# Kernel tuning notes

Hardware: AMD Instinct MI355X
Metric: run time of the kernel (lower is better)

The kernel has to match this reference:

```python
import jax, jax.numpy as jnp
import numpy as np

CS = 64          # chunk_size
CP = CS - 1      # causal_padding
H = 8            # heads
DH = 64          # dim_head
SCALE = DH ** -0.5


def rotate_half(x):
    x1, x2 = jnp.split(x, 2, axis=-1)
    return jnp.concatenate((-x2, x1), axis=-1)


def apply_rope(t, freqs):
    rd = freqs.shape[-1]
    t_rot, t_pass = t[..., :rd], t[..., rd:]
    t_rot = t_rot * jnp.cos(freqs) + rotate_half(t_rot) * jnp.sin(freqs)
    return jnp.concatenate((t_rot, t_pass), axis=-1)


def setup_inputs() -> dict:
    key = jax.random.key(0)
    ks = jax.random.split(key, 10)
    b, n, dim = 4, 4096, 1024
    k_chunks, r, rlen = 64, 2, 128
    inner = H * DH
    return {
        "x": jax.random.normal(ks[0], (b, n, dim), dtype=jnp.float32),
        "context": jax.random.normal(ks[1], (b, k_chunks, r, rlen, dim), dtype=jnp.float32),
        "q_pos_emb": jax.random.normal(ks[2], (1, 1, CS, DH), dtype=jnp.float32),
        "k_pos_emb": jax.random.normal(ks[3], (1, 1, rlen, DH), dtype=jnp.float32),
        "Wq": jax.random.normal(ks[4], (dim, inner), dtype=jnp.float32) * 0.02,
        "Wk": jax.random.normal(ks[5], (dim, inner), dtype=jnp.float32) * 0.02,
        "Wv": jax.random.normal(ks[6], (dim, inner), dtype=jnp.float32) * 0.02,
        "Wo": jax.random.normal(ks[7], (inner, dim), dtype=jnp.float32) * 0.02,
        "bo": jnp.zeros((dim,), dtype=jnp.float32),
        "null_k": jax.random.normal(ks[8], (inner,), dtype=jnp.float32),
        "null_v": jax.random.normal(ks[9], (inner,), dtype=jnp.float32),
    }


def reference(x, context, q_pos_emb, k_pos_emb, Wq, Wk, Wv, Wo, bo, null_k, null_v):
    b, n, dim = x.shape
    _, k_chunks, r, rlen, _ = context.shape
    # causal shift: drop first CP tokens, pad CP zeros at end (F.pad with -CP)
    xs = jnp.pad(x[:, CP:], ((0, 0), (0, CP), (0, 0)))
    seq_index = (n // CS) * CS
    rem = n - seq_index
    xs = xs[:, :seq_index]                                   # [b, k*CS, dim]
    # shift q rope the same way; pad region gets freqs=0 -> identity rotation
    qpe = jnp.pad(q_pos_emb[:, :, CP:], ((0, 0), (0, 0), (0, CP), (0, 0)))
    kpe = jnp.tile(k_pos_emb, (1, 1, r, 1))                  # [1,1,r*rlen,DH]
    bk = b * k_chunks
    xc = xs.reshape(bk, CS, dim)
    ctx = context.reshape(bk, r * rlen, dim)
    # projections -> [bk, h, seq, dh]
    q = (xc @ Wq).reshape(bk, CS, H, DH).transpose(0, 2, 1, 3) * SCALE
    k = (ctx @ Wk).reshape(bk, r * rlen, H, DH).transpose(0, 2, 1, 3)
    v = (ctx @ Wv).reshape(bk, r * rlen, H, DH).transpose(0, 2, 1, 3)
    q = apply_rope(q, qpe)
    k = apply_rope(k, kpe)
    # null kv prepend
    nk = jnp.broadcast_to(null_k.reshape(1, H, 1, DH), (bk, H, 1, DH))
    nv = jnp.broadcast_to(null_v.reshape(1, H, 1, DH), (bk, H, 1, DH))
    k = jnp.concatenate((nk, k), axis=2)
    v = jnp.concatenate((nv, v), axis=2)
    sim = jnp.einsum('bhid,bhjd->bhij', q, k)
    attn = jax.nn.softmax(sim, axis=-1)
    o = jnp.einsum('bhij,bhjd->bhid', attn, v)
    o = o.transpose(0, 2, 1, 3).reshape(bk, CS, H * DH)
    o = o @ Wo + bo                                          # [bk, CS, dim]
    o = o.reshape(b, k_chunks * CS, dim)
    # unshift: pad CP zeros at front, trim CP - rem from end
    o = jnp.concatenate(
        (jnp.zeros((b, CP, dim), o.dtype), o[:, :k_chunks * CS - CP + rem]), axis=1)
    return o
```

## Files before the change

### kernel.cpp

```cpp
#include <hip/hip_runtime.h>


#define DEV __device__ __forceinline__

typedef __bf16 bf16x8 __attribute__((ext_vector_type(8)));
typedef float f32x4 __attribute__((ext_vector_type(4)));

DEV unsigned short f2bf(float f) {
  union { float f; unsigned int u; } v; v.f = f;
  unsigned int u = v.u;
  unsigned int r = (u + 0x7FFFu + ((u >> 16) & 1u)) >> 16;
  return (unsigned short)r;
}
DEV float bf2f(unsigned short h) {
  union { unsigned int u; float f; } v; v.u = ((unsigned int)h) << 16;
  return v.f;
}

DEV void ldst16(const void* g, void* l) {
  __builtin_amdgcn_global_load_lds(
      (const __attribute__((address_space(1))) void*)g,
      (__attribute__((address_space(3))) void*)l, 16, 0, 0);
}


__global__ __launch_bounds__(256) void cast_ctx_k(const float* __restrict__ src,
                                                  unsigned short* __restrict__ dst) {
  size_t i = ((size_t)blockIdx.x * 256 + threadIdx.x) * 8;
  float4 a = *(const float4*)(src + i);
  float4 b = *(const float4*)(src + i + 4);
  union { uint4 v; unsigned short s[8]; } u;
  u.s[0] = f2bf(a.x); u.s[1] = f2bf(a.y); u.s[2] = f2bf(a.z); u.s[3] = f2bf(a.w);
  u.s[4] = f2bf(b.x); u.s[5] = f2bf(b.y); u.s[6] = f2bf(b.z); u.s[7] = f2bf(b.w);
  *(uint4*)(dst + i) = u.v;
}

__global__ __launch_bounds__(256) void cast_x_k(const float* __restrict__ x,
                                                unsigned short* __restrict__ xq) {
  size_t flat = ((size_t)blockIdx.x * 256 + threadIdx.x) * 8;
  int row = (int)(flat >> 10);
  int c = (int)(flat & 1023);
  int b = row >> 12, p = row & 4095;
  union { uint4 v; unsigned short s[8]; } u;
  if (p <= 4032) {
    const float* sp = x + (((size_t)(b << 12) + p + 63) << 10) + c;
    float4 a = *(const float4*)sp;
    float4 d = *(const float4*)(sp + 4);
    u.s[0] = f2bf(a.x); u.s[1] = f2bf(a.y); u.s[2] = f2bf(a.z); u.s[3] = f2bf(a.w);
    u.s[4] = f2bf(d.x); u.s[5] = f2bf(d.y); u.s[6] = f2bf(d.z); u.s[7] = f2bf(d.w);
  } else {
    #pragma unroll
    for (int e = 0; e < 8; ++e) u.s[e] = 0;
  }
  *(uint4*)(xq + flat) = u.v;
}

__global__ __launch_bounds__(256) void transpose_w_k(const float* __restrict__ W,
                                                     unsigned short* __restrict__ Wt,
                                                     int kbits, int N, float scale) {
  int idx = blockIdx.x * 256 + threadIdx.x;
  int K = 1 << kbits;
  int k = idx & (K - 1), n = idx >> kbits;
  Wt[idx] = f2bf(W[(size_t)k * N + n] * scale);
}

__global__ __launch_bounds__(256) void rope_tables_k(const float* __restrict__ qpe,
                                                     const float* __restrict__ kpe,
                                                     float* __restrict__ ck, float* __restrict__ sk,
                                                     float* __restrict__ cq, float* __restrict__ sq) {
  int t = blockIdx.x * 256 + threadIdx.x;
  float f = kpe[t];
  ck[t] = cosf(f);
  sk[t] = sinf(f);
  if (t < 64) {
    float g = qpe[63 * 64 + t];
    cq[t] = cosf(g);
    sq[t] = sinf(g);
  }
}

__global__ __launch_bounds__(256) void rope_k_k(unsigned short* __restrict__ kb,
                                                const float* __restrict__ ck,
                                                const float* __restrict__ sk) {
  size_t t = (size_t)blockIdx.x * 256 + threadIdx.x;
  int m = (int)(t >> 8);
  int rest = (int)(t & 255);
  int h = rest >> 5, dp = rest & 31;
  size_t base = (size_t)m * 512 + h * 64;
  int fi = (m & 127) * 64 + dp;
  float v0 = bf2f(kb[base + dp]);
  float v1 = bf2f(kb[base + dp + 32]);
  float c0 = ck[fi], s0 = sk[fi], c1 = ck[fi + 32], s1 = sk[fi + 32];
  kb[base + dp] = f2bf(v0 * c0 - v1 * s0);
  kb[base + dp + 32] = f2bf(v1 * c1 + v0 * s1);
}

__global__ __launch_bounds__(256) void rope_q_k(unsigned short* __restrict__ qb,
                                                const float* __restrict__ cq,
                                                const float* __restrict__ sq) {
  int t = blockIdx.x * 256 + threadIdx.x;
  int bc = t >> 8, rest = t & 255, h = rest >> 5, dp = rest & 31;
  size_t base = (size_t)(bc * 64) * 512 + h * 64;
  float v0 = bf2f(qb[base + dp]);
  float v1 = bf2f(qb[base + dp + 32]);
  qb[base + dp] = f2bf(v0 * cq[dp] - v1 * sq[dp]);
  qb[base + dp + 32] = f2bf(v1 * cq[dp + 32] + v0 * sq[dp + 32]);
}

__global__ __launch_bounds__(256) void zero_rows_k(float* __restrict__ out) {
  int b = blockIdx.x / 63, rr = blockIdx.x % 63;
  float4 z = {0.f, 0.f, 0.f, 0.f};
  *(float4*)(out + (((size_t)(b * 4096 + rr)) << 10) + threadIdx.x * 4) = z;
}

__global__ __launch_bounds__(256) void gemm_bt(const unsigned short* __restrict__ A,
                                               const unsigned short* __restrict__ B0,
                                               const unsigned short* __restrict__ B1,
                                               unsigned short* __restrict__ C0,
                                               unsigned short* __restrict__ C1,
                                               int M, int N, int K) {
  __shared__ unsigned short As[128 * 64];
  __shared__ unsigned short Bs[128 * 64];
  const unsigned short* B = blockIdx.z ? B1 : B0;
  unsigned short* C = blockIdx.z ? C1 : C0;
  int m0 = blockIdx.x * 128, n0 = blockIdx.y * 128;
  int tid = threadIdx.x, w = tid >> 6, lane = tid & 63;
  int wm = (w & 1) * 64, wn = (w >> 1) * 64;
  int Lrow = lane >> 3, Lc = lane & 7;
  int srcC = Lc ^ (Lrow & 7);

  f32x4 acc[4][4] = {};

  for (int k0 = 0; k0 < K; k0 += 64) {
    #pragma unroll
    for (int q = 0; q < 4; ++q) {
      int t = w * 4 + q;
      ldst16(A + (size_t)(m0 + t * 8 + Lrow) * K + (k0 + srcC * 8), (char*)As + t * 1024);
      ldst16(B + (size_t)(n0 + t * 8 + Lrow) * K + (k0 + srcC * 8), (char*)Bs + t * 1024);
    }
    __syncthreads();
    #pragma unroll
    for (int k32 = 0; k32 < 2; ++k32) {
      int c = k32 * 4 + (lane >> 4);
      bf16x8 af[4], bfr[4];
      #pragma unroll
      for (int mt = 0; mt < 4; ++mt) {
        int m = wm + mt * 16 + (lane & 15);
        af[mt] = *(const bf16x8*)((const char*)As + m * 128 + (c ^ (m & 7)) * 16);
      }
      #pragma unroll
      for (int nt = 0; nt < 4; ++nt) {
        int n = wn + nt * 16 + (lane & 15);
        bfr[nt] = *(const bf16x8*)((const char*)Bs + n * 128 + (c ^ (n & 7)) * 16);
      }
      #pragma unroll
      for (int mt = 0; mt < 4; ++mt)
        #pragma unroll
        for (int nt = 0; nt < 4; ++nt)
          acc[mt][nt] = __builtin_amdgcn_mfma_f32_16x16x32_bf16(af[mt], bfr[nt], acc[mt][nt], 0, 0, 0);
    }
    __syncthreads();
  }
  #pragma unroll
  for (int mt = 0; mt < 4; ++mt)
    #pragma unroll
    for (int nt = 0; nt < 4; ++nt)
      #pragma unroll
      for (int r = 0; r < 4; ++r) {
        int m = m0 + wm + mt * 16 + (lane >> 4) * 4 + r;
        int n = n0 + wn + nt * 16 + (lane & 15);
        C[(size_t)m * N + n] = f2bf(acc[mt][nt][r]);
      }
}

__global__ __launch_bounds__(256) void gemm_out(const unsigned short* __restrict__ A,
                                                const unsigned short* __restrict__ B,
                                                const float* __restrict__ bias,
                                                float* __restrict__ out,
                                                int M, int N, int K) {
  __shared__ unsigned short As[128 * 64];
  __shared__ unsigned short Bs[128 * 64];
  int m0 = blockIdx.x * 128, n0 = blockIdx.y * 128;
  int tid = threadIdx.x, w = tid >> 6, lane = tid & 63;
  int wm = (w & 1) * 64, wn = (w >> 1) * 64;
  int Lrow = lane >> 3, Lc = lane & 7;
  int srcC = Lc ^ (Lrow & 7);

  f32x4 acc[4][4] = {};

  for (int k0 = 0; k0 < K; k0 += 64) {
    #pragma unroll
    for (int q = 0; q < 4; ++q) {
      int t = w * 4 + q;
      ldst16(A + (size_t)(m0 + t * 8 + Lrow) * K + (k0 + srcC * 8), (char*)As + t * 1024);
      ldst16(B + (size_t)(n0 + t * 8 + Lrow) * K + (k0 + srcC * 8), (char*)Bs + t * 1024);
    }
    __syncthreads();
    #pragma unroll
    for (int k32 = 0; k32 < 2; ++k32) {
      int c = k32 * 4 + (lane >> 4);
      bf16x8 af[4], bfr[4];
      #pragma unroll
      for (int mt = 0; mt < 4; ++mt) {
        int m = wm + mt * 16 + (lane & 15);
        af[mt] = *(const bf16x8*)((const char*)As + m * 128 + (c ^ (m & 7)) * 16);
      }
      #pragma unroll
      for (int nt = 0; nt < 4; ++nt) {
        int n = wn + nt * 16 + (lane & 15);
        bfr[nt] = *(const bf16x8*)((const char*)Bs + n * 128 + (c ^ (n & 7)) * 16);
      }
      #pragma unroll
      for (int mt = 0; mt < 4; ++mt)
        #pragma unroll
        for (int nt = 0; nt < 4; ++nt)
          acc[mt][nt] = __builtin_amdgcn_mfma_f32_16x16x32_bf16(af[mt], bfr[nt], acc[mt][nt], 0, 0, 0);
    }
    __syncthreads();
  }
  #pragma unroll
  for (int mt = 0; mt < 4; ++mt)
    #pragma unroll
    for (int nt = 0; nt < 4; ++nt)
      #pragma unroll
      for (int r = 0; r < 4; ++r) {
        int m = m0 + wm + mt * 16 + (lane >> 4) * 4 + r;
        int n = n0 + wn + nt * 16 + (lane & 15);
        int b = m >> 12, t = m & 4095;
        if (t <= 4032)
          out[((size_t)((b << 12) + t + 63)) * N + n] = acc[mt][nt][r] + bias[n];
      }
}

__global__ __launch_bounds__(256) void attn_kernel(const unsigned short* __restrict__ qb,
                                                   const unsigned short* __restrict__ kb,
                                                   const unsigned short* __restrict__ vb,
                                                   const float* __restrict__ nullk,
                                                   const float* __restrict__ nullv,
                                                   unsigned short* __restrict__ ob) {
  __shared__ unsigned short qs[64 * 64];
  __shared__ unsigned short ks[256 * 64];
  __shared__ unsigned short ps[64 * 256];
  __shared__ float rnull[64];
  __shared__ float rsum[64];
  int bc = blockIdx.x, h = blockIdx.y;
  int tid = threadIdx.x, w = tid >> 6, lane = tid & 63;
  int Lrow = lane >> 3, Lc = lane & 7, srcC = Lc ^ (Lrow & 7);

  #pragma unroll
  for (int q8 = 0; q8 < 2; ++q8) {
    int t = w * 2 + q8;
    ldst16(qb + (size_t)(bc * 64 + t * 8 + Lrow) * 512 + h * 64 + srcC * 8, (char*)qs + t * 1024);
  }
  #pragma unroll
  for (int q8 = 0; q8 < 8; ++q8) {
    int t = w * 8 + q8;
    ldst16(kb + (size_t)(bc * 256 + t * 8 + Lrow) * 512 + h * 64 + srcC * 8, (char*)ks + t * 1024);
  }
  __syncthreads();

  {
    int rl = lane >> 2, part = lane & 3;
    int row = w * 16 + rl;
    float s = 0.f;
    #pragma unroll
    for (int e = 0; e < 16; ++e) {
      int d = part * 16 + e;
      unsigned short qv = *(const unsigned short*)((const char*)qs + row * 128 +
                                                   (((d >> 3) ^ (row & 7)) * 16) + (d & 7) * 2);
      s += bf2f(qv) * nullk[h * 64 + d];
    }
    s += __shfl_xor(s, 1);
    s += __shfl_xor(s, 2);
    if (part == 0) rnull[row] = s;
  }

  f32x4 acc[16] = {};
  #pragma unroll
  for (int k32 = 0; k32 < 2; ++k32) {
    int c = k32 * 4 + (lane >> 4);
    int m = w * 16 + (lane & 15);
    bf16x8 a = *(const bf16x8*)((const char*)qs + m * 128 + (c ^ (m & 7)) * 16);
    #pragma unroll
    for (int nt = 0; nt < 16; ++nt) {
      int n = nt * 16 + (lane & 15);
      bf16x8 b = *(const bf16x8*)((const char*)ks + n * 128 + (c ^ (n & 7)) * 16);
      acc[nt] = __builtin_amdgcn_mfma_f32_16x16x32_bf16(a, b, acc[nt], 0, 0, 0);
    }
  }

  int g = lane >> 4;
  #pragma unroll
  for (int r = 0; r < 4; ++r) {
    int row = w * 16 + g * 4 + r;
    float mx = -3.0e38f;
    #pragma unroll
    for (int nt = 0; nt < 16; ++nt) mx = fmaxf(mx, acc[nt][r]);
    mx = fmaxf(mx, __shfl_xor(mx, 1));
    mx = fmaxf(mx, __shfl_xor(mx, 2));
    mx = fmaxf(mx, __shfl_xor(mx, 4));
    mx = fmaxf(mx, __shfl_xor(mx, 8));
    float ns = rnull[row];
    float mm = fmaxf(mx, ns);
    float s = 0.f;
    #pragma unroll
    for (int nt = 0; nt < 16; ++nt) {
      float p = __expf(acc[nt][r] - mm);
      acc[nt][r] = p;
      s += p;
    }
    s += __shfl_xor(s, 1);
    s += __shfl_xor(s, 2);
    s += __shfl_xor(s, 4);
    s += __shfl_xor(s, 8);
    float en = __expf(ns - mm);
    s += en;
    if ((lane & 15) == 0) {
      rsum[row] = s;
      rnull[row] = en;
    }
  }

  #pragma unroll
  for (int nt = 0; nt < 16; ++nt)
    #pragma unroll
    for (int r = 0; r < 4; ++r) {
      int row = w * 16 + g * 4 + r;
      int col = nt * 16 + (lane & 15);
      *(unsigned short*)((char*)ps + row * 512 + (((col >> 3) ^ (row & 7)) * 16) + (col & 7) * 2) =
          f2bf(acc[nt][r]);
    }
  __syncthreads();

  {
    unsigned short* vt = ks;
    const unsigned short* vg = vb + (size_t)(bc * 256 + tid) * 512 + h * 64;
    #pragma unroll
    for (int cc = 0; cc < 8; ++cc) {
      uint4 raw = *(const uint4*)(vg + cc * 8);
      union { uint4 v; unsigned short s[8]; } u;
      u.v = raw;
      #pragma unroll
      for (int e = 0; e < 8; ++e) {
        int d = cc * 8 + e;
        *(unsigned short*)((char*)vt + d * 512 + (((tid >> 3) ^ (d & 7)) * 16) + (tid & 7) * 2) = u.s[e];
      }
    }
  }
  __syncthreads();

  f32x4 oacc[4] = {};
  #pragma unroll
  for (int k32 = 0; k32 < 8; ++k32) {
    int c = k32 * 4 + (lane >> 4);
    int m = w * 16 + (lane & 15);
    bf16x8 a = *(const bf16x8*)((const char*)ps + m * 512 + (c ^ (m & 7)) * 16);
    #pragma unroll
    for (int nt = 0; nt < 4; ++nt) {
      int n = nt * 16 + (lane & 15);
      bf16x8 b = *(const bf16x8*)((const char*)ks + n * 512 + (c ^ (n & 7)) * 16);
      oacc[nt] = __builtin_amdgcn_mfma_f32_16x16x32_bf16(a, b, oacc[nt], 0, 0, 0);
    }
  }
  #pragma unroll
  for (int nt = 0; nt < 4; ++nt)
    #pragma unroll
    for (int r = 0; r < 4; ++r) {
      int row = w * 16 + g * 4 + r;
      int d = nt * 16 + (lane & 15);
      float o = oacc[nt][r] + rnull[row] * nullv[h * 64 + d];
      o /= rsum[row];
      ob[((size_t)(bc * 64 + row) * 8 + h) * 64 + d] = f2bf(o);
    }
}

extern "C" void kernel_launch(void* const* d_in, const int* in_sizes, int n_in,
                              void* d_out, int out_size, void* d_ws, size_t ws_size,
                              hipStream_t stream) {
  const float* x = (const float*)d_in[0];
  const float* ctx = (const float*)d_in[1];
  const float* qpe = (const float*)d_in[2];
  const float* kpe = (const float*)d_in[3];
  const float* Wq = (const float*)d_in[4];
  const float* Wk = (const float*)d_in[5];
  const float* Wv = (const float*)d_in[6];
  const float* Wo = (const float*)d_in[7];
  const float* bo = (const float*)d_in[8];
  const float* nk = (const float*)d_in[9];
  const float* nv = (const float*)d_in[10];
  float* out = (float*)d_out;
  char* ws = (char*)d_ws;

  unsigned short* xq   = (unsigned short*)(ws + 0);
  unsigned short* ctxb = (unsigned short*)(ws + 33554432);
  unsigned short* Wqt  = (unsigned short*)(ws + 167772160);
  unsigned short* Wkt  = (unsigned short*)(ws + 168820736);
  unsigned short* Wvt  = (unsigned short*)(ws + 169869312);
  unsigned short* Wot  = (unsigned short*)(ws + 170917888);
  unsigned short* qb   = (unsigned short*)(ws + 171966464);
  unsigned short* kb   = (unsigned short*)(ws + 188743680);
  unsigned short* vb   = (unsigned short*)(ws + 255852544);
  unsigned short* obuf = (unsigned short*)(ws + 322961408);
  float* cosk = (float*)(ws + 339738624);
  float* sink = (float*)(ws + 339771392);
  float* cosq = (float*)(ws + 339804160);
  float* sinq = (float*)(ws + 339804416);

  zero_rows_k<<<252, 256, 0, stream>>>(out);
  cast_ctx_k<<<32768, 256, 0, stream>>>(ctx, ctxb);
  cast_x_k<<<8192, 256, 0, stream>>>(x, xq);
  transpose_w_k<<<2048, 256, 0, stream>>>(Wq, Wqt, 10, 512, 0.125f);
  transpose_w_k<<<2048, 256, 0, stream>>>(Wk, Wkt, 10, 512, 1.0f);
  transpose_w_k<<<2048, 256, 0, stream>>>(Wv, Wvt, 10, 512, 1.0f);
  transpose_w_k<<<2048, 256, 0, stream>>>(Wo, Wot, 9, 1024, 1.0f);
  rope_tables_k<<<32, 256, 0, stream>>>(qpe, kpe, cosk, sink, cosq, sinq);

  gemm_bt<<<dim3(128, 4, 1), 256, 0, stream>>>(xq, Wqt, Wqt, qb, qb, 16384, 512, 1024);
  gemm_bt<<<dim3(512, 4, 2), 256, 0, stream>>>(ctxb, Wkt, Wvt, kb, vb, 65536, 512, 1024);

  rope_q_k<<<256, 256, 0, stream>>>(qb, cosq, sinq);
  rope_k_k<<<65536, 256, 0, stream>>>(kb, cosk, sink);

  attn_kernel<<<dim3(256, 8), 256, 0, stream>>>(qb, kb, vb, nk, nv, obuf);

  gemm_out<<<dim3(128, 8), 256, 0, stream>>>(obuf, Wot, bo, out, 16384, 1024, 512);
}
```

Measured before the change: 813.3 us.

## Fuse RoPE into projection GEMM epilogues and emit transposed V

Merges the prep kernels (weight transposes, rope tables, zeroing) into one launch and the two casts into another. RoPE for Q and K is now applied in the projection GEMM epilogue, which removes the separate read-modify-write passes over kb and qb. The V projection writes a transposed layout through LDS, so the attention kernel can load V^T with async global-to-LDS copies instead of transposing it with scattered shared stores. Block indices are also remapped, with N-tile-fastest ordering in the GEMMs and grouped chunk/head order in attention, to improve L2 reuse. The cost is strided column writes for transposed V and extra cos/sin table lookups in the epilogue.

After: 804.5 us. Within noise of the previous version (-1.1%).

```diff
diff --git a/kernel.cpp b/kernel.cpp
--- a/kernel.cpp
+++ b/kernel.cpp
@@ -23,107 +23,106 @@
       (__attribute__((address_space(3))) void*)l, 16, 0, 0);
 }
 
-
-__global__ __launch_bounds__(256) void cast_ctx_k(const float* __restrict__ src,
-                                                  unsigned short* __restrict__ dst) {
-  size_t i = ((size_t)blockIdx.x * 256 + threadIdx.x) * 8;
-  float4 a = *(const float4*)(src + i);
-  float4 b = *(const float4*)(src + i + 4);
-  union { uint4 v; unsigned short s[8]; } u;
-  u.s[0] = f2bf(a.x); u.s[1] = f2bf(a.y); u.s[2] = f2bf(a.z); u.s[3] = f2bf(a.w);
-  u.s[4] = f2bf(b.x); u.s[5] = f2bf(b.y); u.s[6] = f2bf(b.z); u.s[7] = f2bf(b.w);
-  *(uint4*)(dst + i) = u.v;
-}
-
-__global__ __launch_bounds__(256) void cast_x_k(const float* __restrict__ x,
-                                                unsigned short* __restrict__ xq) {
-  size_t flat = ((size_t)blockIdx.x * 256 + threadIdx.x) * 8;
-  int row = (int)(flat >> 10);
-  int c = (int)(flat & 1023);
-  int b = row >> 12, p = row & 4095;
-  union { uint4 v; unsigned short s[8]; } u;
-  if (p <= 4032) {
-    const float* sp = x + (((size_t)(b << 12) + p + 63) << 10) + c;
-    float4 a = *(const float4*)sp;
-    float4 d = *(const float4*)(sp + 4);
+__global__ __launch_bounds__(256) void prep_k(const float* __restrict__ Wq,
+                                              const float* __restrict__ Wk,
+                                              const float* __restrict__ Wv,
+                                              const float* __restrict__ Wo,
+                                              const float* __restrict__ qpe,
+                                              const float* __restrict__ kpe,
+                                              unsigned short* __restrict__ Wqt,
+                                              unsigned short* __restrict__ Wkt,
+                                              unsigned short* __restrict__ Wvt,
+                                              unsigned short* __restrict__ Wot,
+                                              float* __restrict__ ck, float* __restrict__ sk,
+                                              float* __restrict__ cq, float* __restrict__ sq,
+                                              float* __restrict__ out) {
+  int blk = blockIdx.x;
+  if (blk < 8192) {
+    int idx = blk * 256 + threadIdx.x;
+    int which = idx >> 19;
+    int loc = idx & 524287;
+    if (which < 3) {
+      int k = loc & 1023, n = loc >> 10;
+      const float* W = which == 0 ? Wq : (which == 1 ? Wk : Wv);
+      unsigned short* Wt = which == 0 ? Wqt : (which == 1 ? Wkt : Wvt);
+      float scale = which == 0 ? 0.125f : 1.0f;
+      Wt[loc] = f2bf(W[(size_t)k * 512 + n] * scale);
+    } else {
+      int k = loc & 511, n = loc >> 9;
+      Wot[loc] = f2bf(Wo[(size_t)k * 1024 + n]);
+    }
+  } else if (blk < 8444) {
+    int r = blk - 8192;
+    int b = r / 63, rr = r % 63;
+    float4 z = {0.f, 0.f, 0.f, 0.f};
+    *(float4*)(out + (((size_t)(b * 4096 + rr)) << 10) + threadIdx.x * 4) = z;
+  } else {
+    int t = (blk - 8444) * 256 + threadIdx.x;
+    float f = kpe[t];
+    ck[t] = cosf(f);
+    sk[t] = sinf(f);
+    if (t < 64) {
+      float g = qpe[63 * 64 + t];
+      cq[t] = cosf(g);
+      sq[t] = sinf(g);
+    }
+  }
+}
+
+__global__ __launch_bounds__(256) void cast_k(const float* __restrict__ ctx,
+                                              const float* __restrict__ x,
+                                              unsigned short* __restrict__ ctxb,
+                                              unsigned short* __restrict__ xq) {
+  int blk = blockIdx.x;
+  if (blk < 32768) {
+    size_t i = ((size_t)blk * 256 + threadIdx.x) * 8;
+    float4 a = *(const float4*)(ctx + i);
+    float4 b = *(const float4*)(ctx + i + 4);
+    union { uint4 v; unsigned short s[8]; } u;
     u.s[0] = f2bf(a.x); u.s[1] = f2bf(a.y); u.s[2] = f2bf(a.z); u.s[3] = f2bf(a.w);
-    u.s[4] = f2bf(d.x); u.s[5] = f2bf(d.y); u.s[6] = f2bf(d.z); u.s[7] = f2bf(d.w);
+    u.s[4] = f2bf(b.x); u.s[5] = f2bf(b.y); u.s[6] = f2bf(b.z); u.s[7] = f2bf(b.w);
+    *(uint4*)(ctxb + i) = u.v;
   } else {
-    #pragma unroll
-    for (int e = 0; e < 8; ++e) u.s[e] = 0;
-  }
-  *(uint4*)(xq + flat) = u.v;
-}
-
-__global__ __launch_bounds__(256) void transpose_w_k(const float* __restrict__ W,
-                                                     unsigned short* __restrict__ Wt,
-                                                     int kbits, int N, float scale) {
-  int idx = blockIdx.x * 256 + threadIdx.x;
-  int K = 1 << kbits;
-  int k = idx & (K - 1), n = idx >> kbits;
-  Wt[idx] = f2bf(W[(size_t)k * N + n] * scale);
-}
-
-__global__ __launch_bounds__(256) void rope_tables_k(const float* __restrict__ qpe,
-                                                     const float* __restrict__ kpe,
-                                                     float* __restrict__ ck, float* __restrict__ sk,
-                                                     float* __restrict__ cq, float* __restrict__ sq) {
-  int t = blockIdx.x * 256 + threadIdx.x;
-  float f = kpe[t];
-  ck[t] = cosf(f);
-  sk[t] = sinf(f);
-  if (t < 64) {
-    float g = qpe[63 * 64 + t];
-    cq[t] = cosf(g);
-    sq[t] = sinf(g);
-  }
-}
-
-__global__ __launch_bounds__(256) void rope_k_k(unsigned short* __restrict__ kb,
-                                                const float* __restrict__ ck,
-                                                const float* __restrict__ sk) {
-  size_t t = (size_t)blockIdx.x * 256 + threadIdx.x;
-  int m = (int)(t >> 8);
-  int rest = (int)(t & 255);
-  int h = rest >> 5, dp = rest & 31;
-  size_t base = (size_t)m * 512 + h * 64;
-  int fi = (m & 127) * 64 + dp;
-  float v0 = bf2f(kb[base + dp]);
-  float v1 = bf2f(kb[base + dp + 32]);
-  float c0 = ck[fi], s0 = sk[fi], c1 = ck[fi + 32], s1 = sk[fi + 32];
-  kb[base + dp] = f2bf(v0 * c0 - v1 * s0);
-  kb[base + dp + 32] = f2bf(v1 * c1 + v0 * s1);
-}
-
-__global__ __launch_bounds__(256) void rope_q_k(unsigned short* __restrict__ qb,
-                                                const float* __restrict__ cq,
-                                                const float* __restrict__ sq) {
-  int t = blockIdx.x * 256 + threadIdx.x;
-  int bc = t >> 8, rest = t & 255, h = rest >> 5, dp = rest & 31;
-  size_t base = (size_t)(bc * 64) * 512 + h * 64;
-  float v0 = bf2f(qb[base + dp]);
-  float v1 = bf2f(qb[base + dp + 32]);
-  qb[base + dp] = f2bf(v0 * cq[dp] - v1 * sq[dp]);
-  qb[base + dp + 32] = f2bf(v1 * cq[dp + 32] + v0 * sq[dp + 32]);
-}
-
-__global__ __launch_bounds__(256) void zero_rows_k(float* __restrict__ out) {
-  int b = blockIdx.x / 63, rr = blockIdx.x % 63;
-  float4 z = {0.f, 0.f, 0.f, 0.f};
-  *(float4*)(out + (((size_t)(b * 4096 + rr)) << 10) + threadIdx.x * 4) = z;
-}
-
-__global__ __launch_bounds__(256) void gemm_bt(const unsigned short* __restrict__ A,
-                                               const unsigned short* __restrict__ B0,
-                                               const unsigned short* __restrict__ B1,
-                                               unsigned short* __restrict__ C0,
-                                               unsigned short* __restrict__ C1,
-                                               int M, int N, int K) {
-  __shared__ unsigned short As[128 * 64];
-  __shared__ unsigned short Bs[128 * 64];
-  const unsigned short* B = blockIdx.z ? B1 : B0;
-  unsigned short* C = blockIdx.z ? C1 : C0;
-  int m0 = blockIdx.x * 128, n0 = blockIdx.y * 128;
+    size_t flat = ((size_t)(blk - 32768) * 256 + threadIdx.x) * 8;
+    int row = (int)(flat >> 10);
+    int c = (int)(flat & 1023);
+    int b = row >> 12, p = row & 4095;
+    union { uint4 v; unsigned short s[8]; } u;
+    if (p <= 4032) {
+      const float* sp = x + (((size_t)(b << 12) + p + 63) << 10) + c;
+      float4 a = *(const float4*)sp;
+      float4 d = *(const float4*)(sp + 4);
+      u.s[0] = f2bf(a.x); u.s[1] = f2bf(a.y); u.s[2] = f2bf(a.z); u.s[3] = f2bf(a.w);
+      u.s[4] = f2bf(d.x); u.s[5] = f2bf(d.y); u.s[6] = f2bf(d.z); u.s[7] = f2bf(d.w);
+    } else {
+      #pragma unroll
+      for (int e = 0; e < 8; ++e) u.s[e] = 0;
+    }
+    *(uint4*)(xq + flat) = u.v;
+  }
+}
+
+template <int MODE>
+__global__ __launch_bounds__(256) void gemm_proj(const unsigned short* __restrict__ A,
+                                                 const unsigned short* __restrict__ B0,
+                                                 const unsigned short* __restrict__ B1,
+                                                 unsigned short* __restrict__ out0,
+                                                 unsigned short* __restrict__ out1,
+                                                 const float* __restrict__ ck,
+                                                 const float* __restrict__ sk,
+                                                 const float* __restrict__ cq,
+                                                 const float* __restrict__ sq,
+                                                 int M, int K) {
+  __shared__ unsigned short sh[16384];
+  unsigned short* As = sh;
+  unsigned short* Bs = sh + 8192;
+
+  int id = blockIdx.x;
+  int x, y, z;
+  if (MODE == 0) { y = id & 3; x = id >> 2; z = 0; }
+  else           { y = id & 3; z = (id >> 2) & 1; x = id >> 3; }
+  const unsigned short* B = z ? B1 : B0;
+  int m0 = x * 128, n0 = y * 128;
   int tid = threadIdx.x, w = tid >> 6, lane = tid & 63;
   int wm = (w & 1) * 64, wn = (w >> 1) * 64;
   int Lrow = lane >> 3, Lc = lane & 7;
@@ -161,26 +160,75 @@
     }
     __syncthreads();
   }
-  #pragma unroll
-  for (int mt = 0; mt < 4; ++mt)
-    #pragma unroll
-    for (int nt = 0; nt < 4; ++nt)
+
+  if (MODE == 0) {
+    #pragma unroll
+    for (int mt = 0; mt < 4; ++mt)
+      #pragma unroll
+      for (int nt = 0; nt < 4; ++nt)
+        #pragma unroll
+        for (int r = 0; r < 4; ++r) {
+          int m = m0 + wm + mt * 16 + (lane >> 4) * 4 + r;
+          int n = n0 + wn + nt * 16 + (lane & 15);
+          float val = acc[mt][nt][r];
+          if ((m & 63) == 0) {
+            int d = nt * 16 + (lane & 15);
+            float partner = acc[mt][nt ^ 2][r];
+            val = val * cq[d] + (nt < 2 ? -partner : partner) * sq[d];
+          }
+          out0[(size_t)m * 512 + n] = f2bf(val);
+        }
+  } else if (z == 0) {
+    #pragma unroll
+    for (int mt = 0; mt < 4; ++mt)
       #pragma unroll
       for (int r = 0; r < 4; ++r) {
         int m = m0 + wm + mt * 16 + (lane >> 4) * 4 + r;
-        int n = n0 + wn + nt * 16 + (lane & 15);
-        C[(size_t)m * N + n] = f2bf(acc[mt][nt][r]);
-      }
+        int fib = (m & 127) * 64;
+        #pragma unroll
+        for (int nt = 0; nt < 4; ++nt) {
+          int n = n0 + wn + nt * 16 + (lane & 15);
+          int d = nt * 16 + (lane & 15);
+          float partner = acc[mt][nt ^ 2][r];
+          float val = acc[mt][nt][r] * ck[fib + d] + (nt < 2 ? -partner : partner) * sk[fib + d];
+          out0[(size_t)m * 512 + n] = f2bf(val);
+        }
+      }
+  } else {
+    #pragma unroll
+    for (int mt = 0; mt < 4; ++mt)
+      #pragma unroll
+      for (int nt = 0; nt < 4; ++nt)
+        #pragma unroll
+        for (int r = 0; r < 4; ++r) {
+          int ml = wm + mt * 16 + (lane >> 4) * 4 + r;
+          int nl = wn + nt * 16 + (lane & 15);
+          int mc = ml >> 3, me = ml & 7;
+          *(unsigned short*)((char*)sh + nl * 256 + ((mc ^ (nl & 15)) * 16) + me * 2) =
+              f2bf(acc[mt][nt][r]);
+        }
+    __syncthreads();
+    #pragma unroll
+    for (int i = 0; i < 8; ++i) {
+      int flat = i * 256 + tid;
+      int nl = flat >> 4, mc = flat & 15;
+      uint4 v = *(const uint4*)((const char*)sh + nl * 256 + ((mc ^ (nl & 15)) * 16));
+      *(uint4*)(out1 + (size_t)(n0 + nl) * M + m0 + mc * 8) = v;
+    }
+  }
 }
 
 __global__ __launch_bounds__(256) void gemm_out(const unsigned short* __restrict__ A,
                                                 const unsigned short* __restrict__ B,
                                                 const float* __restrict__ bias,
-                                                float* __restrict__ out,
-                                                int M, int N, int K) {
-  __shared__ unsigned short As[128 * 64];
-  __shared__ unsigned short Bs[128 * 64];
-  int m0 = blockIdx.x * 128, n0 = blockIdx.y * 128;
+                                                float* __restrict__ out) {
+  __shared__ unsigned short sh[16384];
+  unsigned short* As = sh;
+  unsigned short* Bs = sh + 8192;
+  const int K = 512, N = 1024;
+  int id = blockIdx.x;
+  int y = id & 7, x = id >> 3;
+  int m0 = x * 128, n0 = y * 128;
   int tid = threadIdx.x, w = tid >> 6, lane = tid & 63;
   int wm = (w & 1) * 64, wn = (w >> 1) * 64;
   int Lrow = lane >> 3, Lc = lane & 7;
@@ -234,7 +282,7 @@
 
 __global__ __launch_bounds__(256) void attn_kernel(const unsigned short* __restrict__ qb,
                                                    const unsigned short* __restrict__ kb,
-                                                   const unsigned short* __restrict__ vb,
+                                                   const unsigned short* __restrict__ vtg,
                                                    const float* __restrict__ nullk,
                                                    const float* __restrict__ nullv,
                                                    unsigned short* __restrict__ ob) {
@@ -243,7 +291,9 @@
   __shared__ unsigned short ps[64 * 256];
   __shared__ float rnull[64];
   __shared__ float rsum[64];
-  int bc = blockIdx.x, h = blockIdx.y;
+  int id = blockIdx.x;
+  int bc = (id & 7) + 8 * (id >> 6);
+  int h = (id >> 3) & 7;
   int tid = threadIdx.x, w = tid >> 6, lane = tid & 63;
   int Lrow = lane >> 3, Lc = lane & 7, srcC = Lc ^ (Lrow & 7);
 
@@ -332,20 +382,12 @@
     }
   __syncthreads();
 
-  {
-    unsigned short* vt = ks;
-    const unsigned short* vg = vb + (size_t)(bc * 256 + tid) * 512 + h * 64;
-    #pragma unroll
-    for (int cc = 0; cc < 8; ++cc) {
-      uint4 raw = *(const uint4*)(vg + cc * 8);
-      union { uint4 v; unsigned short s[8]; } u;
-      u.v = raw;
-      #pragma unroll
-      for (int e = 0; e < 8; ++e) {
-        int d = cc * 8 + e;
-        *(unsigned short*)((char*)vt + d * 512 + (((tid >> 3) ^ (d & 7)) * 16) + (tid & 7) * 2) = u.s[e];
-      }
-    }
+  #pragma unroll
+  for (int q8 = 0; q8 < 8; ++q8) {
+    int t = w * 8 + q8;
+    int dd = t * 2 + (lane >> 5);
+    int cl = (lane & 31) ^ (dd & 7);
+    ldst16(vtg + (size_t)(h * 64 + dd) * 65536 + bc * 256 + cl * 8, (char*)ks + t * 1024);
   }
   __syncthreads();
 
@@ -399,29 +441,23 @@
   unsigned short* Wot  = (unsigned short*)(ws + 170917888);
   unsigned short* qb   = (unsigned short*)(ws + 171966464);
   unsigned short* kb   = (unsigned short*)(ws + 188743680);
-  unsigned short* vb   = (unsigned short*)(ws + 255852544);
+  unsigned short* vtg  = (unsigned short*)(ws + 255852544);
   unsigned short* obuf = (unsigned short*)(ws + 322961408);
   float* cosk = (float*)(ws + 339738624);
   float* sink = (float*)(ws + 339771392);
   float* cosq = (float*)(ws + 339804160);
   float* sinq = (float*)(ws + 339804416);
 
-  zero_rows_k<<<252, 256, 0, stream>>>(out);
-  cast_ctx_k<<<32768, 256, 0, stream>>>(ctx, ctxb);
-  cast_x_k<<<8192, 256, 0, stream>>>(x, xq);
-  transpose_w_k<<<2048, 256, 0, stream>>>(Wq, Wqt, 10, 512, 0.125f);
-  transpose_w_k<<<2048, 256, 0, stream>>>(Wk, Wkt, 10, 512, 1.0f);
-  transpose_w_k<<<2048, 256, 0, stream>>>(Wv, Wvt, 10, 512, 1.0f);
-  transpose_w_k<<<2048, 256, 0, stream>>>(Wo, Wot, 9, 1024, 1.0f);
-  rope_tables_k<<<32, 256, 0, stream>>>(qpe, kpe, cosk, sink, cosq, sinq);
-
-  gemm_bt<<<dim3(128, 4, 1), 256, 0, stream>>>(xq, Wqt, Wqt, qb, qb, 16384, 512, 1024);
-  gemm_bt<<<dim3(512, 4, 2), 256, 0, stream>>>(ctxb, Wkt, Wvt, kb, vb, 65536, 512, 1024);
-
-  rope_q_k<<<256, 256, 0, stream>>>(qb, cosq, sinq);
-  rope_k_k<<<65536, 256, 0, stream>>>(kb, cosk, sink);
-
-  attn_kernel<<<dim3(256, 8), 256, 0, stream>>>(qb, kb, vb, nk, nv, obuf);
-
-  gemm_out<<<dim3(128, 8), 256, 0, stream>>>(obuf, Wot, bo, out, 16384, 1024, 512);
-}
+  prep_k<<<8476, 256, 0, stream>>>(Wq, Wk, Wv, Wo, qpe, kpe, Wqt, Wkt, Wvt, Wot,
+                                   cosk, sink, cosq, sinq, out);
+  cast_k<<<40960, 256, 0, stream>>>(ctx, x, ctxb, xq);
+
+  gemm_proj<0><<<512, 256, 0, stream>>>(xq, Wqt, Wqt, qb, nullptr,
+                                        cosk, sink, cosq, sinq, 16384, 1024);
+  gemm_proj<1><<<4096, 256, 0, stream>>>(ctxb, Wkt, Wvt, kb, vtg,
+                                         cosk, sink, cosq, sinq, 65536, 1024);
+
+  attn_kernel<<<2048, 256, 0, stream>>>(qb, kb, vtg, nk, nv, obuf);
+
+  gemm_out<<<1024, 256, 0, stream>>>(obuf, Wot, bo, out);
+}
```
